# Optimization experiments

Measured on AMD Instinct MI355X. Metric: run time of the kernel, lower is better.

Reference implementation:

```python
import jax, jax.numpy as jnp
import numpy as np

EMBED = 1024
HEADS = 16
HEAD_DIM = EMBED // HEADS


def setup_inputs() -> dict:
    key = jax.random.key(0)
    ks = jax.random.split(key, 8)
    N, S = 4, 2048
    return {
        "keys": jax.random.normal(ks[0], (N, S, EMBED), dtype=jnp.float32),
        "query": jax.random.normal(ks[1], (N, S, EMBED), dtype=jnp.float32),
        "values": jax.random.normal(ks[2], (N, S, EMBED), dtype=jnp.float32),
        "Wk": jax.random.normal(ks[3], (HEAD_DIM, HEAD_DIM), dtype=jnp.float32) / np.sqrt(HEAD_DIM),
        "Wq": jax.random.normal(ks[4], (HEAD_DIM, HEAD_DIM), dtype=jnp.float32) / np.sqrt(HEAD_DIM),
        "Wv": jax.random.normal(ks[5], (HEAD_DIM, HEAD_DIM), dtype=jnp.float32) / np.sqrt(HEAD_DIM),
        "Wo": jax.random.normal(ks[6], (EMBED, EMBED), dtype=jnp.float32) / np.sqrt(EMBED),
        "bo": jax.random.normal(ks[7], (EMBED,), dtype=jnp.float32) * 0.01,
    }


def reference(keys, query, values, Wk, Wq, Wv, Wo, bo):
    N, Q, _ = query.shape
    K = keys.shape[1]
    # split heads: [n, s, h, d]
    k = keys.reshape(N, K, HEADS, HEAD_DIM) @ Wk.T
    q = query.reshape(N, Q, HEADS, HEAD_DIM) @ Wq.T
    v = values.reshape(N, K, HEADS, HEAD_DIM) @ Wv.T
    energy = jnp.einsum("nqhd,nkhd->nhqk", q, k)
    # NOTE: original torch code scales by embed_size**1 / 2 == embed_size/2 (quirk, kept faithful)
    attention = jax.nn.softmax(energy / (EMBED / 2), axis=3)
    out = jnp.einsum("nhqk,nkhd->nqhd", attention, v).reshape(N, Q, EMBED)
    return out @ Wo.T + bo
```

## Files before the change

### kernel.cpp

```cpp
#include <hip/hip_runtime.h>
#include <hip/hip_bf16.h>

#define HEADS 16
#define HDIM 64
#define EMB 1024
#define NBATCH 4
#define SEQ 2048
#define NT (SEQ/64)

typedef __bf16 bf16x8 __attribute__((ext_vector_type(8)));
typedef __bf16 bf16x4 __attribute__((ext_vector_type(4)));
typedef float f32x4 __attribute__((ext_vector_type(4)));
typedef float f32x16 __attribute__((ext_vector_type(16)));

#define Z16 {0.f,0.f,0.f,0.f,0.f,0.f,0.f,0.f,0.f,0.f,0.f,0.f,0.f,0.f,0.f,0.f}

static __device__ __forceinline__ bf16x8 load_cvt8(const float* __restrict__ p) {
    float4 a = *reinterpret_cast<const float4*>(p);
    float4 b = *reinterpret_cast<const float4*>(p + 4);
    bf16x8 r;
    r[0] = (__bf16)a.x; r[1] = (__bf16)a.y; r[2] = (__bf16)a.z; r[3] = (__bf16)a.w;
    r[4] = (__bf16)b.x; r[5] = (__bf16)b.y; r[6] = (__bf16)b.z; r[7] = (__bf16)b.w;
    return r;
}

static __device__ __forceinline__ unsigned cvt_pk_bf16(float a, float b) {
    unsigned d;
    asm("v_cvt_pk_bf16_f32 %0, %1, %2" : "=v"(d) : "v"(a), "v"(b));
    return d;
}

static __device__ __forceinline__ void pl_swap(unsigned &a, unsigned &b) {
#if __has_builtin(__builtin_amdgcn_permlane32_swap)
    auto r = __builtin_amdgcn_permlane32_swap((int)a, (int)b, false, false);
    a = (unsigned)r[0]; b = (unsigned)r[1];
#else
    asm("v_permlane32_swap_b32 %0, %1" : "+v"(a), "+v"(b));
#endif
}

__global__ __launch_bounds__(256) void proj_kernel(
    const float* __restrict__ keys, const float* __restrict__ query,
    const float* __restrict__ values,
    const float* __restrict__ Wk, const float* __restrict__ Wq,
    const float* __restrict__ Wv, const float* __restrict__ Wo,
    __bf16* __restrict__ qb, __bf16* __restrict__ kb, __bf16* __restrict__ vtb,
    __bf16* __restrict__ wob)
{
    int t = threadIdx.x;
    int which = blockIdx.z;

    if (which == 3) {
        int idx = blockIdx.y*gridDim.x + blockIdx.x;
        if (idx < EMB*EMB/4/256) {
            int i = idx*256 + t;
            float4 v = reinterpret_cast<const float4*>(Wo)[i];
            bf16x4 r;
            r[0] = (__bf16)v.x; r[1] = (__bf16)v.y; r[2] = (__bf16)v.z; r[3] = (__bf16)v.w;
            reinterpret_cast<bf16x4*>(wob)[i] = r;
        }
        return;
    }

    __shared__ __align__(16) __bf16 vlds[64][72];

    int wave = t >> 6, lane = t & 63;
    int l16 = lane & 15, g = lane >> 4;
    int sblk = blockIdx.x, nh = blockIdx.y;
    int n = nh >> 4, h = nh & 15;

    const float* X = (which == 0) ? query : (which == 1) ? keys : values;
    const float* W = (which == 0) ? Wq    : (which == 1) ? Wk   : Wv;
    const float wsc = (which == 0) ? (1.44269504088896f / 512.f) : 1.0f;

    {
        const float* wp = W + t*16;
        int row = t >> 2, c0 = (t & 3)*16;
#pragma unroll
        for (int q4 = 0; q4 < 4; ++q4) {
            float4 v = *reinterpret_cast<const float4*>(wp + q4*4);
            vlds[row][c0 + q4*4 + 0] = (__bf16)(v.x*wsc);
            vlds[row][c0 + q4*4 + 1] = (__bf16)(v.y*wsc);
            vlds[row][c0 + q4*4 + 2] = (__bf16)(v.z*wsc);
            vlds[row][c0 + q4*4 + 3] = (__bf16)(v.w*wsc);
        }
    }
    __syncthreads();

    bf16x8 wf[4][2];
#pragma unroll
    for (int j = 0; j < 4; ++j)
#pragma unroll
        for (int kc = 0; kc < 2; ++kc)
            wf[j][kc] = *reinterpret_cast<const bf16x8*>(&vlds[j*16 + l16][kc*32 + g*8]);

    int s0 = sblk*64 + wave*16;
    const float* xp = X + ((size_t)(n*SEQ + s0 + l16)*HEADS + h)*64;
    bf16x8 af0 = load_cvt8(xp + g*8);
    bf16x8 af1 = load_cvt8(xp + 32 + g*8);

    __syncthreads();

    f32x4 acc[4];
#pragma unroll
    for (int j = 0; j < 4; ++j) acc[j] = (f32x4){0.f, 0.f, 0.f, 0.f};
#pragma unroll
    for (int j = 0; j < 4; ++j) {
        acc[j] = __builtin_amdgcn_mfma_f32_16x16x32_bf16(af0, wf[j][0], acc[j], 0, 0, 0);
        acc[j] = __builtin_amdgcn_mfma_f32_16x16x32_bf16(af1, wf[j][1], acc[j], 0, 0, 0);
    }

#pragma unroll
    for (int j = 0; j < 4; ++j)
#pragma unroll
        for (int r = 0; r < 4; ++r)
            vlds[wave*16 + g*4 + r][j*16 + l16] = (__bf16)acc[j][r];
    __syncthreads();

    if (which < 2) {
        int row = t >> 2, seg = t & 3;
        __bf16* dst = (which == 0 ? qb : kb) + (size_t)nh*SEQ*64
                      + (size_t)(sblk*64 + row)*64 + seg*16;
        *reinterpret_cast<int4*>(dst)     = *reinterpret_cast<const int4*>(&vlds[row][seg*16]);
        *reinterpret_cast<int4*>(dst + 8) = *reinterpret_cast<const int4*>(&vlds[row][seg*16 + 8]);
    } else {
        int d = t & 63, sc4 = t >> 6;
        alignas(16) __bf16 tmp[16];
#pragma unroll
        for (int i = 0; i < 16; ++i) tmp[i] = vlds[sc4*16 + i][d];
        __bf16* dst = vtb + ((size_t)nh*64 + d)*SEQ + sblk*64 + sc4*16;
        *reinterpret_cast<int4*>(dst)     = *reinterpret_cast<const int4*>(tmp);
        *reinterpret_cast<int4*>(dst + 8) = *reinterpret_cast<const int4*>(tmp + 8);
    }
}

__global__ __launch_bounds__(256, 2) void attn_kernel(
    const __bf16* __restrict__ qb, const __bf16* __restrict__ kb,
    const __bf16* __restrict__ vtb, __bf16* __restrict__ ob)
{
    __shared__ __align__(16) char smem[65536];

    int t = threadIdx.x;
    int wave = t >> 6, lane = t & 63;
    int l31 = lane & 31, hi = lane >> 5;

    int id = blockIdx.x;
    int qblk = id >> 6;
    int nh = (id & 7)*8 + ((id >> 3) & 7);
    int n = nh >> 4, h = nh & 15;

    const __bf16* Qp = qb  + (size_t)nh*SEQ*64;
    const __bf16* Kp = kb  + (size_t)nh*SEQ*64;
    const __bf16* Vp = vtb + (size_t)nh*64*SEQ;

    int st_row[2], st_col[2];
#pragma unroll
    for (int i = 0; i < 2; ++i) {
        int o = wave*2048 + i*1024 + lane*16;
        st_row[i] = o >> 7;
        st_col[i] = (o & 127) ^ ((st_row[i] & 7) << 4);
    }

    int q0 = qblk*256 + wave*64;
    const __bf16* qp = Qp + (size_t)(q0 + l31)*64 + hi*8;
    bf16x8 qfA[4], qfB[4];
#pragma unroll
    for (int i = 0; i < 4; ++i) {
        qfA[i] = *reinterpret_cast<const bf16x8*>(qp + i*16);
        qfB[i] = *reinterpret_cast<const bf16x8*>(qp + 2048 + i*16);
    }

    f32x16 oaccA0 = Z16, oaccA1 = Z16, oaccB0 = Z16, oaccB1 = Z16;
    float lsA0 = 0.f, lsA1 = 0.f, lsA2 = 0.f, lsA3 = 0.f;
    float lsB0 = 0.f, lsB1 = 0.f, lsB2 = 0.f, lsB3 = 0.f;

#define STAGE_TILE(gbase, stride, ldsoff)                                          \
    {                                                                              \
        _Pragma("unroll")                                                          \
        for (int i_ = 0; i_ < 2; ++i_) {                                           \
            const char* g_ = (const char*)((gbase) + (size_t)st_row[i_]*(stride))  \
                             + st_col[i_];                                         \
            __builtin_amdgcn_global_load_lds(                                      \
                (const __attribute__((address_space(1))) void*)g_,                 \
                (__attribute__((address_space(3))) void*)(smem + (ldsoff)          \
                    + wave*2048 + i_*1024), 16, 0, 0);                             \
        }                                                                          \
    }

#define QKT2()                                                                     \
    {                                                                              \
        bf16x8 k00_ = *(const bf16x8*)(kb_ + (l31)*128      + ((0*32 + hi*16) ^ swz)); \
        bf16x8 k01_ = *(const bf16x8*)(kb_ + (l31)*128      + ((1*32 + hi*16) ^ swz)); \
        bf16x8 k02_ = *(const bf16x8*)(kb_ + (l31)*128      + ((2*32 + hi*16) ^ swz)); \
        bf16x8 k03_ = *(const bf16x8*)(kb_ + (l31)*128      + ((3*32 + hi*16) ^ swz)); \
        bf16x8 k10_ = *(const bf16x8*)(kb_ + (32 + l31)*128 + ((0*32 + hi*16) ^ swz)); \
        bf16x8 k11_ = *(const bf16x8*)(kb_ + (32 + l31)*128 + ((1*32 + hi*16) ^ swz)); \
        bf16x8 k12_ = *(const bf16x8*)(kb_ + (32 + l31)*128 + ((2*32 + hi*16) ^ swz)); \
        bf16x8 k13_ = *(const bf16x8*)(kb_ + (32 + l31)*128 + ((3*32 + hi*16) ^ swz)); \
        __builtin_amdgcn_s_setprio(1);                                             \
        eA0 = __builtin_amdgcn_mfma_f32_32x32x16_bf16(k00_, qfA[0], eA0, 0, 0, 0); \
        eB0 = __builtin_amdgcn_mfma_f32_32x32x16_bf16(k00_, qfB[0], eB0, 0, 0, 0); \
        eA1 = __builtin_amdgcn_mfma_f32_32x32x16_bf16(k10_, qfA[0], eA1, 0, 0, 0); \
        eB1 = __builtin_amdgcn_mfma_f32_32x32x16_bf16(k10_, qfB[0], eB1, 0, 0, 0); \
        eA0 = __builtin_amdgcn_mfma_f32_32x32x16_bf16(k01_, qfA[1], eA0, 0, 0, 0); \
        eB0 = __builtin_amdgcn_mfma_f32_32x32x16_bf16(k01_, qfB[1], eB0, 0, 0, 0); \
        eA1 = __builtin_amdgcn_mfma_f32_32x32x16_bf16(k11_, qfA[1], eA1, 0, 0, 0); \
        eB1 = __builtin_amdgcn_mfma_f32_32x32x16_bf16(k11_, qfB[1], eB1, 0, 0, 0); \
        eA0 = __builtin_amdgcn_mfma_f32_32x32x16_bf16(k02_, qfA[2], eA0, 0, 0, 0); \
        eB0 = __builtin_amdgcn_mfma_f32_32x32x16_bf16(k02_, qfB[2], eB0, 0, 0, 0); \
        eA1 = __builtin_amdgcn_mfma_f32_32x32x16_bf16(k12_, qfA[2], eA1, 0, 0, 0); \
        eB1 = __builtin_amdgcn_mfma_f32_32x32x16_bf16(k12_, qfB[2], eB1, 0, 0, 0); \
        eA0 = __builtin_amdgcn_mfma_f32_32x32x16_bf16(k03_, qfA[3], eA0, 0, 0, 0); \
        eB0 = __builtin_amdgcn_mfma_f32_32x32x16_bf16(k03_, qfB[3], eB0, 0, 0, 0); \
        eA1 = __builtin_amdgcn_mfma_f32_32x32x16_bf16(k13_, qfA[3], eA1, 0, 0, 0); \
        eB1 = __builtin_amdgcn_mfma_f32_32x32x16_bf16(k13_, qfB[3], eB1, 0, 0, 0); \
        __builtin_amdgcn_s_setprio(0);                                             \
    }

#define MAKE_PU_FAST(E, P, PU0, PU1)                                               \
    {                                                                              \
        _Pragma("unroll")                                                          \
        for (int i_ = 0; i_ < 16; ++i_)                                            \
            P[i_] = __builtin_amdgcn_exp2f(E[i_]);                                 \
        unsigned w00 = cvt_pk_bf16(P[0],  P[1]);                                   \
        unsigned w01 = cvt_pk_bf16(P[2],  P[3]);                                   \
        unsigned w10 = cvt_pk_bf16(P[4],  P[5]);                                   \
        unsigned w11 = cvt_pk_bf16(P[6],  P[7]);                                   \
        unsigned w20 = cvt_pk_bf16(P[8],  P[9]);                                   \
        unsigned w21 = cvt_pk_bf16(P[10], P[11]);                                  \
        unsigned w30 = cvt_pk_bf16(P[12], P[13]);                                  \
        unsigned w31 = cvt_pk_bf16(P[14], P[15]);                                  \
        pl_swap(w00, w10); pl_swap(w01, w11);                                      \
        pl_swap(w20, w30); pl_swap(w21, w31);                                      \
        PU0.u[0] = w00; PU0.u[1] = w01; PU0.u[2] = w10; PU0.u[3] = w11;            \
        PU1.u[0] = w20; PU1.u[1] = w21; PU1.u[2] = w30; PU1.u[3] = w31;            \
    }

#define LS_ACC(P, LS0, LS1, LS2, LS3)                                              \
    {                                                                              \
        LS0 += P[0] + P[4];  LS1 += P[1] + P[5];                                   \
        LS2 += P[2] + P[6];  LS3 += P[3] + P[7];                                   \
        LS0 += P[8] + P[12]; LS1 += P[9] + P[13];                                  \
        LS2 += P[10] + P[14]; LS3 += P[11] + P[15];                                \
    }

#define SMPV(SB, EA, EB)                                                           \
    {                                                                              \
        union { unsigned u[4]; bf16x8 v; } puA0, puA1, puB0, puB1;                 \
        float pA_[16], pB_[16];                                                    \
        MAKE_PU_FAST(EA, pA_, puA0, puA1)                                          \
        MAKE_PU_FAST(EB, pB_, puB0, puB1)                                          \
        bf16x8 v00 = *(const bf16x8*)(vb_ + (l31)*128      + (((SB)*64 +  0 + hi*16) ^ swz)); \
        bf16x8 v01 = *(const bf16x8*)(vb_ + (l31)*128      + (((SB)*64 + 32 + hi*16) ^ swz)); \
        bf16x8 v10 = *(const bf16x8*)(vb_ + (32 + l31)*128 + (((SB)*64 +  0 + hi*16) ^ swz)); \
        bf16x8 v11 = *(const bf16x8*)(vb_ + (32 + l31)*128 + (((SB)*64 + 32 + hi*16) ^ swz)); \
        __builtin_amdgcn_s_setprio(1);                                             \
        oaccA0 = __builtin_amdgcn_mfma_f32_32x32x16_bf16(v00, puA0.v, oaccA0, 0, 0, 0); \
        oaccA1 = __builtin_amdgcn_mfma_f32_32x32x16_bf16(v10, puA0.v, oaccA1, 0, 0, 0); \
        oaccB0 = __builtin_amdgcn_mfma_f32_32x32x16_bf16(v00, puB0.v, oaccB0, 0, 0, 0); \
        oaccB1 = __builtin_amdgcn_mfma_f32_32x32x16_bf16(v10, puB0.v, oaccB1, 0, 0, 0); \
        oaccA0 = __builtin_amdgcn_mfma_f32_32x32x16_bf16(v01, puA1.v, oaccA0, 0, 0, 0); \
        oaccA1 = __builtin_amdgcn_mfma_f32_32x32x16_bf16(v11, puA1.v, oaccA1, 0, 0, 0); \
        oaccB0 = __builtin_amdgcn_mfma_f32_32x32x16_bf16(v01, puB1.v, oaccB0, 0, 0, 0); \
        oaccB1 = __builtin_amdgcn_mfma_f32_32x32x16_bf16(v11, puB1.v, oaccB1, 0, 0, 0); \
        __builtin_amdgcn_s_setprio(0);                                             \
        LS_ACC(pA_, lsA0, lsA1, lsA2, lsA3)                                        \
        LS_ACC(pB_, lsB0, lsB1, lsB2, lsB3)                                        \
    }

    STAGE_TILE(Kp, 64, 0);
    STAGE_TILE(Vp, SEQ, 32768);
    STAGE_TILE(Kp + (size_t)64*64, 64, 8192);
    STAGE_TILE(Vp + 64, SEQ, 32768 + 8192);

    for (int kt = 0; kt < NT; ++kt) {
        if (kt + 2 < NT) {
            int b2 = (kt + 2) & 3;
            const __bf16* knext = Kp + (size_t)(kt + 2)*64*64;
            const __bf16* vnext = Vp + (size_t)(kt + 2)*64;
            STAGE_TILE(knext, 64, b2*8192);
            STAGE_TILE(vnext, SEQ, 32768 + b2*8192);
        }
        if (kt < NT - 2)       asm volatile("s_waitcnt vmcnt(8)" ::: "memory");
        else if (kt == NT - 2) asm volatile("s_waitcnt vmcnt(4)" ::: "memory");
        else                   asm volatile("s_waitcnt vmcnt(0)" ::: "memory");
        __builtin_amdgcn_s_barrier();
        __builtin_amdgcn_sched_barrier(0);

        const char* kb_ = smem + (kt & 3)*8192;
        const char* vb_ = smem + 32768 + (kt & 3)*8192;
        int swz = (l31 & 7) << 4;

        f32x16 eA0 = Z16, eB0 = Z16, eA1 = Z16, eB1 = Z16;
        QKT2()
        __builtin_amdgcn_sched_barrier(0);
        SMPV(0, eA0, eB0)
        SMPV(1, eA1, eB1)
        __builtin_amdgcn_sched_barrier(0);
    }

    float lA = (lsA0 + lsA1) + (lsA2 + lsA3);
    float totA = lA + __shfl_xor(lA, 32);
    float invA = 1.f / totA;
    float lB = (lsB0 + lsB1) + (lsB2 + lsB3);
    float totB = lB + __shfl_xor(lB, 32);
    float invB = 1.f / totB;

    __bf16* opA = ob + (size_t)(n*SEQ + q0 + l31)*EMB + h*64;
    __bf16* opB = opA + (size_t)32*EMB;
#pragma unroll
    for (int j = 0; j < 4; ++j)
#pragma unroll
        for (int c = 0; c < 4; ++c) {
            int d_ = c + 8*j + 4*hi;
            opA[d_]      = (__bf16)(oaccA0[4*j + c] * invA);
            opA[32 + d_] = (__bf16)(oaccA1[4*j + c] * invA);
            opB[d_]      = (__bf16)(oaccB0[4*j + c] * invB);
            opB[32 + d_] = (__bf16)(oaccB1[4*j + c] * invB);
        }
#undef STAGE_TILE
#undef QKT2
#undef MAKE_PU_FAST
#undef LS_ACC
#undef SMPV
}

__global__ __launch_bounds__(256, 2) void out_gemm_kernel(
    const __bf16* __restrict__ ob, const __bf16* __restrict__ wob,
    const float* __restrict__ bo, float* __restrict__ out)
{
    __shared__ __align__(16) char smem[65536];

    int t = threadIdx.x;
    int wave = t >> 6, lane = t & 63;
    int l16 = lane & 15, g = lane >> 4;

    int bid = blockIdx.x;
    int swz = (bid & 7)*64 + (bid >> 3);
    int mb = (swz >> 3)*128;
    int nb = (swz & 7)*128;
    int wr = wave >> 1, wc = wave & 1;

    int st_row[4], st_col[4];
#pragma unroll
    for (int i = 0; i < 4; ++i) {
        int o = i*4096 + wave*1024 + lane*16;
        st_row[i] = o >> 7;
        st_col[i] = (o & 127) ^ ((st_row[i] & 7) << 4);
    }

#define G_STAGE(kt, buf)                                                            \
    {                                                                               \
        _Pragma("unroll")                                                           \
        for (int i_ = 0; i_ < 4; ++i_) {                                            \
            const char* ga_ = (const char*)(ob + (size_t)(mb + st_row[i_])*EMB      \
                                + (kt)*64) + st_col[i_];                            \
            __builtin_amdgcn_global_load_lds(                                       \
                (const __attribute__((address_space(1))) void*)ga_,                 \
                (__attribute__((address_space(3))) void*)(smem + (buf)*16384        \
                    + i_*4096 + wave*1024), 16, 0, 0);                              \
            const char* gb_ = (const char*)(wob + (size_t)(nb + st_row[i_])*EMB     \
                                + (kt)*64) + st_col[i_];                            \
            __builtin_amdgcn_global_load_lds(                                       \
                (const __attribute__((address_space(1))) void*)gb_,                 \
                (__attribute__((address_space(3))) void*)(smem + 32768 + (buf)*16384\
                    + i_*4096 + wave*1024), 16, 0, 0);                              \
        }                                                                           \
    }

    f32x4 acc[4][4];
#pragma unroll
    for (int m = 0; m < 4; ++m)
#pragma unroll
        for (int n = 0; n < 4; ++n) acc[m][n] = (f32x4){0.f, 0.f, 0.f, 0.f};

    G_STAGE(0, 0);
    __syncthreads();

    int cur = 0;
    for (int kt = 0; kt < EMB/64; ++kt) {
        if (kt + 1 < EMB/64) G_STAGE(kt + 1, cur ^ 1);

        const char* ab_ = smem + cur*16384;
        const char* bb_ = smem + 32768 + cur*16384;

        bf16x8 af[4][2], bf[4][2];
#pragma unroll
        for (int m = 0; m < 4; ++m) {
            int row = wr*64 + m*16 + l16, s = (row & 7) << 4;
            af[m][0] = *(const bf16x8*)(ab_ + row*128 + ((g*16) ^ s));
            af[m][1] = *(const bf16x8*)(ab_ + row*128 + ((64 + g*16) ^ s));
        }
#pragma unroll
        for (int n = 0; n < 4; ++n) {
            int row = wc*64 + n*16 + l16, s = (row & 7) << 4;
            bf[n][0] = *(const bf16x8*)(bb_ + row*128 + ((g*16) ^ s));
            bf[n][1] = *(const bf16x8*)(bb_ + row*128 + ((64 + g*16) ^ s));
        }

        __builtin_amdgcn_s_setprio(1);
#pragma unroll
        for (int m = 0; m < 4; ++m)
#pragma unroll
            for (int n = 0; n < 4; ++n) {
                acc[m][n] = __builtin_amdgcn_mfma_f32_16x16x32_bf16(af[m][0], bf[n][0], acc[m][n], 0, 0, 0);
                acc[m][n] = __builtin_amdgcn_mfma_f32_16x16x32_bf16(af[m][1], bf[n][1], acc[m][n], 0, 0, 0);
            }
        __builtin_amdgcn_s_setprio(0);

        __syncthreads();
        cur ^= 1;
    }

#pragma unroll
    for (int n = 0; n < 4; ++n) {
        int col = nb + wc*64 + n*16 + l16;
        float bias = bo[col];
#pragma unroll
        for (int m = 0; m < 4; ++m) {
            int rowb = mb + wr*64 + m*16 + g*4;
#pragma unroll
            for (int r = 0; r < 4; ++r)
                out[(size_t)(rowb + r)*EMB + col] = acc[m][n][r] + bias;
        }
    }
#undef G_STAGE
}

extern "C" void kernel_launch(void* const* d_in, const int* in_sizes, int n_in,
                              void* d_out, int out_size, void* d_ws, size_t ws_size,
                              hipStream_t stream) {
    const float* keys   = (const float*)d_in[0];
    const float* query  = (const float*)d_in[1];
    const float* values = (const float*)d_in[2];
    const float* Wk     = (const float*)d_in[3];
    const float* Wq     = (const float*)d_in[4];
    const float* Wv     = (const float*)d_in[5];
    const float* Wo     = (const float*)d_in[6];
    const float* bo     = (const float*)d_in[7];
    float* out = (float*)d_out;

    char* ws = (char*)d_ws;
    __bf16* qb  = (__bf16*)(ws);
    __bf16* kb  = (__bf16*)(ws + (size_t)16*1024*1024);
    __bf16* vtb = (__bf16*)(ws + (size_t)32*1024*1024);
    __bf16* ob  = (__bf16*)(ws + (size_t)48*1024*1024);
    __bf16* wob = (__bf16*)(ws + (size_t)64*1024*1024);

    hipLaunchKernelGGL(proj_kernel, dim3(SEQ/64, NBATCH*HEADS, 4), dim3(256), 0, stream,
                       keys, query, values, Wk, Wq, Wv, Wo, qb, kb, vtb, wob);
    hipLaunchKernelGGL(attn_kernel, dim3(512), dim3(256), 0, stream,
                       qb, kb, vtb, ob);
    hipLaunchKernelGGL(out_gemm_kernel, dim3(512), dim3(256), 0, stream,
                       ob, wob, bo, out);
}
```

Measured before the change: 129.3 us.

## Software-pipeline QK^T of next tile with softmax/PV of current tile

Restructures the attention main loop into a two-stage software pipeline: QK^T for tile t+1 is issued in the same iteration as the exp/PV work for tile t, using ping-pong score registers (x/y), and the loop is unrolled by two. The goal is to overlap MFMA work with the exp2/conversion VALU work and hide the dependency between score computation and softmax. The first MFMA of each QK^T chain now takes a constant zero accumulator instead of a freshly zeroed register, so the separate zero-initialisation disappears. In exchange register pressure rises because two sets of score accumulators stay live, which could cause spills or lower occupancy at launch bounds of 2, and the prologue and epilogue logic is more complex.

```diff
diff --git a/kernel.cpp b/kernel.cpp
--- a/kernel.cpp
+++ b/kernel.cpp
@@ -170,9 +170,15 @@
         qfB[i] = *reinterpret_cast<const bf16x8*>(qp + 2048 + i*16);
     }
 
+    const f32x16 vzero = Z16;
     f32x16 oaccA0 = Z16, oaccA1 = Z16, oaccB0 = Z16, oaccB1 = Z16;
     float lsA0 = 0.f, lsA1 = 0.f, lsA2 = 0.f, lsA3 = 0.f;
     float lsB0 = 0.f, lsB1 = 0.f, lsB2 = 0.f, lsB3 = 0.f;
+
+    f32x16 xA0, xA1, xB0, xB1;
+    f32x16 yA0, yA1, yB0, yB1;
+    const char *kb_, *vb_;
+    int swz = (l31 & 7) << 4;
 
 #define STAGE_TILE(gbase, stride, ldsoff)                                          \
     {                                                                              \
@@ -187,7 +193,14 @@
         }                                                                          \
     }
 
-#define QKT2()                                                                     \
+#define STAGE(s)                                                                   \
+    {                                                                              \
+        int b_ = (s) & 3;                                                          \
+        STAGE_TILE(Kp + (size_t)(s)*64*64, 64, b_*8192);                           \
+        STAGE_TILE(Vp + (size_t)(s)*64, SEQ, 32768 + b_*8192);                     \
+    }
+
+#define QKT2(EA0, EB0, EA1, EB1)                                                   \
     {                                                                              \
         bf16x8 k00_ = *(const bf16x8*)(kb_ + (l31)*128      + ((0*32 + hi*16) ^ swz)); \
         bf16x8 k01_ = *(const bf16x8*)(kb_ + (l31)*128      + ((1*32 + hi*16) ^ swz)); \
@@ -198,22 +211,22 @@
         bf16x8 k12_ = *(const bf16x8*)(kb_ + (32 + l31)*128 + ((2*32 + hi*16) ^ swz)); \
         bf16x8 k13_ = *(const bf16x8*)(kb_ + (32 + l31)*128 + ((3*32 + hi*16) ^ swz)); \
         __builtin_amdgcn_s_setprio(1);                                             \
-        eA0 = __builtin_amdgcn_mfma_f32_32x32x16_bf16(k00_, qfA[0], eA0, 0, 0, 0); \
-        eB0 = __builtin_amdgcn_mfma_f32_32x32x16_bf16(k00_, qfB[0], eB0, 0, 0, 0); \
-        eA1 = __builtin_amdgcn_mfma_f32_32x32x16_bf16(k10_, qfA[0], eA1, 0, 0, 0); \
-        eB1 = __builtin_amdgcn_mfma_f32_32x32x16_bf16(k10_, qfB[0], eB1, 0, 0, 0); \
-        eA0 = __builtin_amdgcn_mfma_f32_32x32x16_bf16(k01_, qfA[1], eA0, 0, 0, 0); \
-        eB0 = __builtin_amdgcn_mfma_f32_32x32x16_bf16(k01_, qfB[1], eB0, 0, 0, 0); \
-        eA1 = __builtin_amdgcn_mfma_f32_32x32x16_bf16(k11_, qfA[1], eA1, 0, 0, 0); \
-        eB1 = __builtin_amdgcn_mfma_f32_32x32x16_bf16(k11_, qfB[1], eB1, 0, 0, 0); \
-        eA0 = __builtin_amdgcn_mfma_f32_32x32x16_bf16(k02_, qfA[2], eA0, 0, 0, 0); \
-        eB0 = __builtin_amdgcn_mfma_f32_32x32x16_bf16(k02_, qfB[2], eB0, 0, 0, 0); \
-        eA1 = __builtin_amdgcn_mfma_f32_32x32x16_bf16(k12_, qfA[2], eA1, 0, 0, 0); \
-        eB1 = __builtin_amdgcn_mfma_f32_32x32x16_bf16(k12_, qfB[2], eB1, 0, 0, 0); \
-        eA0 = __builtin_amdgcn_mfma_f32_32x32x16_bf16(k03_, qfA[3], eA0, 0, 0, 0); \
-        eB0 = __builtin_amdgcn_mfma_f32_32x32x16_bf16(k03_, qfB[3], eB0, 0, 0, 0); \
-        eA1 = __builtin_amdgcn_mfma_f32_32x32x16_bf16(k13_, qfA[3], eA1, 0, 0, 0); \
-        eB1 = __builtin_amdgcn_mfma_f32_32x32x16_bf16(k13_, qfB[3], eB1, 0, 0, 0); \
+        EA0 = __builtin_amdgcn_mfma_f32_32x32x16_bf16(k00_, qfA[0], vzero, 0, 0, 0); \
+        EB0 = __builtin_amdgcn_mfma_f32_32x32x16_bf16(k00_, qfB[0], vzero, 0, 0, 0); \
+        EA1 = __builtin_amdgcn_mfma_f32_32x32x16_bf16(k10_, qfA[0], vzero, 0, 0, 0); \
+        EB1 = __builtin_amdgcn_mfma_f32_32x32x16_bf16(k10_, qfB[0], vzero, 0, 0, 0); \
+        EA0 = __builtin_amdgcn_mfma_f32_32x32x16_bf16(k01_, qfA[1], EA0, 0, 0, 0); \
+        EB0 = __builtin_amdgcn_mfma_f32_32x32x16_bf16(k01_, qfB[1], EB0, 0, 0, 0); \
+        EA1 = __builtin_amdgcn_mfma_f32_32x32x16_bf16(k11_, qfA[1], EA1, 0, 0, 0); \
+        EB1 = __builtin_amdgcn_mfma_f32_32x32x16_bf16(k11_, qfB[1], EB1, 0, 0, 0); \
+        EA0 = __builtin_amdgcn_mfma_f32_32x32x16_bf16(k02_, qfA[2], EA0, 0, 0, 0); \
+        EB0 = __builtin_amdgcn_mfma_f32_32x32x16_bf16(k02_, qfB[2], EB0, 0, 0, 0); \
+        EA1 = __builtin_amdgcn_mfma_f32_32x32x16_bf16(k12_, qfA[2], EA1, 0, 0, 0); \
+        EB1 = __builtin_amdgcn_mfma_f32_32x32x16_bf16(k12_, qfB[2], EB1, 0, 0, 0); \
+        EA0 = __builtin_amdgcn_mfma_f32_32x32x16_bf16(k03_, qfA[3], EA0, 0, 0, 0); \
+        EB0 = __builtin_amdgcn_mfma_f32_32x32x16_bf16(k03_, qfB[3], EB0, 0, 0, 0); \
+        EA1 = __builtin_amdgcn_mfma_f32_32x32x16_bf16(k13_, qfA[3], EA1, 0, 0, 0); \
+        EB1 = __builtin_amdgcn_mfma_f32_32x32x16_bf16(k13_, qfB[3], EB1, 0, 0, 0); \
         __builtin_amdgcn_s_setprio(0);                                             \
     }
 
@@ -268,36 +281,52 @@
         LS_ACC(pB_, lsB0, lsB1, lsB2, lsB3)                                        \
     }
 
-    STAGE_TILE(Kp, 64, 0);
-    STAGE_TILE(Vp, SEQ, 32768);
-    STAGE_TILE(Kp + (size_t)64*64, 64, 8192);
-    STAGE_TILE(Vp + 64, SEQ, 32768 + 8192);
-
-    for (int kt = 0; kt < NT; ++kt) {
-        if (kt + 2 < NT) {
-            int b2 = (kt + 2) & 3;
-            const __bf16* knext = Kp + (size_t)(kt + 2)*64*64;
-            const __bf16* vnext = Vp + (size_t)(kt + 2)*64;
-            STAGE_TILE(knext, 64, b2*8192);
-            STAGE_TILE(vnext, SEQ, 32768 + b2*8192);
-        }
-        if (kt < NT - 2)       asm volatile("s_waitcnt vmcnt(8)" ::: "memory");
-        else if (kt == NT - 2) asm volatile("s_waitcnt vmcnt(4)" ::: "memory");
-        else                   asm volatile("s_waitcnt vmcnt(0)" ::: "memory");
+    STAGE(0);
+    STAGE(1);
+
+    asm volatile("s_waitcnt vmcnt(4)" ::: "memory");
+    __builtin_amdgcn_s_barrier();
+    __builtin_amdgcn_sched_barrier(0);
+    STAGE(2);
+    kb_ = smem + 0*8192;
+    QKT2(xA0, xB0, xA1, xB1)
+
+    for (int p = 0; p < 15; ++p) {
+        int t1 = 2*p + 1;
+        asm volatile("s_waitcnt vmcnt(4)" ::: "memory");
         __builtin_amdgcn_s_barrier();
         __builtin_amdgcn_sched_barrier(0);
-
-        const char* kb_ = smem + (kt & 3)*8192;
-        const char* vb_ = smem + 32768 + (kt & 3)*8192;
-        int swz = (l31 & 7) << 4;
-
-        f32x16 eA0 = Z16, eB0 = Z16, eA1 = Z16, eB1 = Z16;
-        QKT2()
+        STAGE(t1 + 2);
+        kb_ = smem + (t1 & 3)*8192;
+        vb_ = smem + 32768 + ((t1 - 1) & 3)*8192;
+        QKT2(yA0, yB0, yA1, yB1)
+        SMPV(0, xA0, xB0)
+        SMPV(1, xA1, xB1)
+
+        int t2 = t1 + 1;
+        asm volatile("s_waitcnt vmcnt(4)" ::: "memory");
+        __builtin_amdgcn_s_barrier();
         __builtin_amdgcn_sched_barrier(0);
-        SMPV(0, eA0, eB0)
-        SMPV(1, eA1, eB1)
-        __builtin_amdgcn_sched_barrier(0);
-    }
+        if (t2 + 2 < NT) STAGE(t2 + 2);
+        kb_ = smem + (t2 & 3)*8192;
+        vb_ = smem + 32768 + ((t2 - 1) & 3)*8192;
+        QKT2(xA0, xB0, xA1, xB1)
+        SMPV(0, yA0, yB0)
+        SMPV(1, yA1, yB1)
+    }
+
+    asm volatile("s_waitcnt vmcnt(0)" ::: "memory");
+    __builtin_amdgcn_s_barrier();
+    __builtin_amdgcn_sched_barrier(0);
+    kb_ = smem + (31 & 3)*8192;
+    vb_ = smem + 32768 + ((31 - 1) & 3)*8192;
+    QKT2(yA0, yB0, yA1, yB1)
+    SMPV(0, xA0, xB0)
+    SMPV(1, xA1, xB1)
+
+    vb_ = smem + 32768 + (31 & 3)*8192;
+    SMPV(0, yA0, yB0)
+    SMPV(1, yA1, yB1)
 
     float lA = (lsA0 + lsA1) + (lsA2 + lsA3);
     float totA = lA + __shfl_xor(lA, 32);
@@ -319,6 +348,7 @@
             opB[32 + d_] = (__bf16)(oaccB1[4*j + c] * invB);
         }
 #undef STAGE_TILE
+#undef STAGE
 #undef QKT2
 #undef MAKE_PU_FAST
 #undef LS_ACC
```

New measurement: 194.5 us. 50.5% more time.
